# Performance work log

Measured on AMD Instinct MI355X. Metric: run time of the kernel, lower is better.

Reference implementation:

```python
import jax, jax.numpy as jnp
import numpy as np

B, N, IN_DIM, HID = 32, 1024, 128, 64


def setup_inputs() -> dict:
    key = jax.random.key(0)
    ks = jax.random.split(key, 12)
    s_in = 1.0 / np.sqrt(IN_DIM)
    s_h = 1.0 / np.sqrt(HID)
    return {
        "x": jax.random.normal(ks[0], (B, N, IN_DIM), dtype=jnp.float32),
        "A": jax.random.uniform(ks[1], (B, N, N), dtype=jnp.float32),
        # fc_hidden: input_dim -> hidden_dim
        "W_h": jax.random.uniform(ks[2], (IN_DIM, HID), jnp.float32, -s_in, s_in),
        "b_h": jax.random.uniform(ks[3], (HID,), jnp.float32, -s_in, s_in),
        # fc_1 inside Gated_Skip_Connection (input_dim != output_dim)
        "W_fc1": jax.random.uniform(ks[4], (IN_DIM, HID), jnp.float32, -s_in, s_in),
        "b_fc1": jax.random.uniform(ks[5], (HID,), jnp.float32, -s_in, s_in),
        # gated_X1, gated_X2: hidden -> hidden
        "W_g1": jax.random.uniform(ks[6], (HID, HID), jnp.float32, -s_h, s_h),
        "b_g1": jax.random.uniform(ks[7], (HID,), jnp.float32, -s_h, s_h),
        "W_g2": jax.random.uniform(ks[8], (HID, HID), jnp.float32, -s_h, s_h),
        "b_g2": jax.random.uniform(ks[9], (HID,), jnp.float32, -s_h, s_h),
    }


def reference(x, A, W_h, b_h, W_fc1, b_fc1, W_g1, b_g1, W_g2, b_g2):
    # x_new = bmm(A, fc_hidden(x))   [B, N, HID]
    x_new = jnp.einsum("bnm,bmh->bnh", A, x @ W_h + b_h)
    # gated skip connection (input_dim != output_dim -> project x first)
    x_proj = x @ W_fc1 + b_fc1
    gate = jax.nn.sigmoid((x_proj @ W_g1 + b_g1) + (x_new @ W_g2 + b_g2))
    out = x_new * gate + x_proj * (1.0 - gate)
    return out
```

## Files before the change

### kernel.cpp

```cpp
#include <hip/hip_runtime.h>
#include <hip/hip_bf16.h>

#define NB 32
#define NN 1024
#define IND 128
#define HD 64

typedef float f32x4 __attribute__((ext_vector_type(4)));
typedef short bf16x8 __attribute__((ext_vector_type(8)));
typedef unsigned short ushortx4 __attribute__((ext_vector_type(4)));

union FragU { unsigned short us[8]; bf16x8 v; };

__device__ __forceinline__ unsigned short f2bf(float f) {
    union { float f; unsigned u; } x; x.f = f;
    unsigned r = x.u + 0x7FFFu + ((x.u >> 16) & 1u);
    return (unsigned short)(r >> 16);
}
__device__ __forceinline__ float bf2f(unsigned short h) {
    union { unsigned u; float f; } x; x.u = ((unsigned)h) << 16; return x.f;
}

__device__ __forceinline__ void gl16(void* lds, const void* g) {
    __builtin_amdgcn_global_load_lds(
        (const __attribute__((address_space(1))) unsigned int*)g,
        (__attribute__((address_space(3))) unsigned int*)lds, 16, 0, 0);
}

__global__ void prep_k(const float* __restrict__ W_h, const float* __restrict__ W_fc1,
                       const float* __restrict__ W_g1, const float* __restrict__ W_g2,
                       const float* __restrict__ b_g1, const float* __restrict__ b_g2,
                       unsigned short* __restrict__ WcT_hi, unsigned short* __restrict__ WcT_lo,
                       unsigned short* __restrict__ Wg1T_hi, unsigned short* __restrict__ Wg1T_lo,
                       unsigned short* __restrict__ Wg2T_hi, unsigned short* __restrict__ Wg2T_lo,
                       float* __restrict__ biasP1) {
    int t = blockIdx.x * blockDim.x + threadIdx.x;
    if (t < 16384) {
        int o = t >> 7, k = t & 127;
        float v = (o < 64) ? W_h[k * 64 + o] : W_fc1[k * 64 + (o - 64)];
        unsigned short hi = f2bf(v);
        WcT_hi[t] = hi; WcT_lo[t] = f2bf(v - bf2f(hi));
    } else if (t < 20480) {
        int r = t - 16384; int o = r >> 6, k = r & 63;
        float v = W_g1[k * 64 + o];
        unsigned short hi = f2bf(v);
        Wg1T_hi[r] = hi; Wg1T_lo[r] = f2bf(v - bf2f(hi));
    } else if (t < 24576) {
        int r = t - 20480; int o = r >> 6, k = r & 63;
        float v = W_g2[k * 64 + o];
        unsigned short hi = f2bf(v);
        Wg2T_hi[r] = hi; Wg2T_lo[r] = f2bf(v - bf2f(hi));
    } else if (t < 24640) {
        int j = t - 24576;
        biasP1[j] = b_g1[j] + b_g2[j];
    }
}

__global__ __launch_bounds__(64) void k1(
        const float* __restrict__ x,
        const unsigned short* __restrict__ WcT_hi, const unsigned short* __restrict__ WcT_lo,
        const unsigned short* __restrict__ Wg1T_hi, const unsigned short* __restrict__ Wg1T_lo,
        const float* __restrict__ b_h, const float* __restrict__ b_fc1,
        const float* __restrict__ biasP1,
        unsigned short* __restrict__ hF, float* __restrict__ xproj,
        float* __restrict__ p1) {
    __shared__ unsigned short lds_hi[16 * 64];
    __shared__ unsigned short lds_lo[16 * 64];

    const int lane = threadIdx.x;
    const int lr = lane & 15, lg = lane >> 4;
    const int blk = blockIdx.x;
    const int b = blk >> 6;
    const int n0 = (blk & 63) * 16;

    const float* xp = x + (size_t)(b * NN + n0 + lr) * IND;

    f32x4 xa[4][2];
#pragma unroll
    for (int ks = 0; ks < 4; ks++) {
        const f32x4* ap = (const f32x4*)(xp + 32 * ks + 8 * lg);
        xa[ks][0] = ap[0]; xa[ks][1] = ap[1];
    }

    f32x4 acc[8];
#pragma unroll
    for (int f = 0; f < 8; f++) acc[f] = (f32x4){0.f, 0.f, 0.f, 0.f};

#pragma unroll
    for (int ks = 0; ks < 4; ks++) {
        FragU ah, al;
#pragma unroll
        for (int i = 0; i < 4; i++) {
            unsigned short h0 = f2bf(xa[ks][0][i]); ah.us[i] = h0;     al.us[i]     = f2bf(xa[ks][0][i] - bf2f(h0));
            unsigned short h1 = f2bf(xa[ks][1][i]); ah.us[4 + i] = h1; al.us[4 + i] = f2bf(xa[ks][1][i] - bf2f(h1));
        }
#pragma unroll
        for (int f = 0; f < 8; f++) {
            int off = (16 * f + lr) * 128 + 32 * ks + 8 * lg;
            bf16x8 wh = *(const bf16x8*)(WcT_hi + off);
            bf16x8 wl = *(const bf16x8*)(WcT_lo + off);
            acc[f] = __builtin_amdgcn_mfma_f32_16x16x32_bf16(ah.v, wh, acc[f], 0, 0, 0);
            acc[f] = __builtin_amdgcn_mfma_f32_16x16x32_bf16(ah.v, wl, acc[f], 0, 0, 0);
            acc[f] = __builtin_amdgcn_mfma_f32_16x16x32_bf16(al.v, wh, acc[f], 0, 0, 0);
        }
    }

    const int mb = n0 + 4 * lg;
    const int tile = mb >> 5;
    const int lanepart = lr + 16 * ((mb >> 3) & 3);
    const int j0 = mb & 7;

#pragma unroll
    for (int f = 0; f < 4; f++) {
        int c = 16 * f + lr;
        float bh = b_h[c];
        ushortx4 hv;
#pragma unroll
        for (int r = 0; r < 4; r++) hv[r] = f2bf(acc[f][r] + bh);
        *(ushortx4*)(hF + (size_t)b * 65536 + (size_t)(tile * 4 + f) * 512 + lanepart * 8 + j0) = hv;
    }

#pragma unroll
    for (int f = 4; f < 8; f++) {
        int c = 16 * (f - 4) + lr;
        float bp = b_fc1[c];
#pragma unroll
        for (int r = 0; r < 4; r++) {
            float v = acc[f][r] + bp;
            int n = mb + r;
            xproj[(size_t)(b * NN + n) * 64 + c] = v;
            int ln = 4 * lg + r;
            int idx = ln * 64 + (((c >> 3) ^ (ln & 7)) << 3) + (c & 7);
            unsigned short hi = f2bf(v);
            lds_hi[idx] = hi;
            lds_lo[idx] = f2bf(v - bf2f(hi));
        }
    }
    __syncthreads();

    f32x4 accP[4];
#pragma unroll
    for (int f = 0; f < 4; f++) accP[f] = (f32x4){0.f, 0.f, 0.f, 0.f};
#pragma unroll
    for (int ks = 0; ks < 2; ks++) {
        int c0 = 32 * ks + 8 * lg;
        int idx = lr * 64 + (((c0 >> 3) ^ (lr & 7)) << 3);
        bf16x8 a_hi = *(const bf16x8*)(lds_hi + idx);
        bf16x8 a_lo = *(const bf16x8*)(lds_lo + idx);
#pragma unroll
        for (int f = 0; f < 4; f++) {
            int off = (16 * f + lr) * 64 + c0;
            bf16x8 b_hi = *(const bf16x8*)(Wg1T_hi + off);
            bf16x8 b_lo = *(const bf16x8*)(Wg1T_lo + off);
            accP[f] = __builtin_amdgcn_mfma_f32_16x16x32_bf16(a_hi, b_hi, accP[f], 0, 0, 0);
            accP[f] = __builtin_amdgcn_mfma_f32_16x16x32_bf16(a_hi, b_lo, accP[f], 0, 0, 0);
            accP[f] = __builtin_amdgcn_mfma_f32_16x16x32_bf16(a_lo, b_hi, accP[f], 0, 0, 0);
        }
    }
#pragma unroll
    for (int f = 0; f < 4; f++) {
        int c = 16 * f + lr;
        float bb = biasP1[c];
#pragma unroll
        for (int r = 0; r < 4; r++) {
            int n = mb + r;
            p1[(size_t)(b * NN + n) * 64 + c] = accP[f][r] + bb;
        }
    }
}

__global__ __launch_bounds__(256, 4) void k2(
        const float* __restrict__ A, const unsigned short* __restrict__ hF,
        const unsigned short* __restrict__ Wg2T_hi, const unsigned short* __restrict__ Wg2T_lo,
        const float* __restrict__ p1, const float* __restrict__ xproj,
        float* __restrict__ out) {
    __shared__ char smem[32768];

    const int tid = threadIdx.x;
    const int w = tid >> 6, lane = tid & 63;
    const int lr = lane & 15, lg = lane >> 4;

    const int bid = blockIdx.x;
    const int wgid = (bid & 7) * 256 + (bid >> 3);
    const int b = wgid >> 6;
    const int strip = wgid & 63;

    const float* aS[4];
#pragma unroll
    for (int i = 0; i < 4; i++) {
        int rl = w * 4 + i;
        aS[i] = A + (size_t)(b * NN + strip * 16 + rl) * NN + ((lane ^ rl) << 2);
    }
    const unsigned short* hp = hF + (size_t)b * 65536 + w * 512 + lane * 8;

    f32x4 acc = (f32x4){0.f, 0.f, 0.f, 0.f};
    bf16x8 hb[8];

#pragma unroll
    for (int i = 0; i < 4; i++)
        gl16(smem + (w * 4 + i) * 1024, aS[i]);
#pragma unroll
    for (int ks = 0; ks < 8; ks++)
        hb[ks] = *(const bf16x8*)(hp + (size_t)ks * 2048);
    __syncthreads();

#define COMPUTE(ks, Abase)                                                     \
    {                                                                          \
        int g0 = (ks) * 8 + lg * 2;                                            \
        f32x4 a0 = *(const f32x4*)((Abase) + ((g0 ^ lr) << 4));                \
        f32x4 a1 = *(const f32x4*)((Abase) + (((g0 + 1) ^ lr) << 4));          \
        FragU au;                                                              \
        _Pragma("unroll")                                                      \
        for (int ii = 0; ii < 4; ii++) {                                       \
            au.us[ii] = f2bf(a0[ii]); au.us[4 + ii] = f2bf(a1[ii]);            \
        }                                                                      \
        acc = __builtin_amdgcn_mfma_f32_16x16x32_bf16(au.v, hb[ks], acc, 0, 0, 0); \
    }

#pragma unroll
    for (int t = 0; t < 4; t++) {
        const int slot = t & 1;
        const char* Abase = smem + slot * 16384 + lr * 1024;

        if (t < 3) {
#pragma unroll
            for (int i = 0; i < 4; i++)
                gl16(smem + (slot ^ 1) * 16384 + (w * 4 + i) * 1024,
                     aS[i] + (t + 1) * 256);
        }

        COMPUTE(0, Abase) COMPUTE(1, Abase) COMPUTE(2, Abase) COMPUTE(3, Abase)
        if (t < 3) {
#pragma unroll
            for (int ks = 0; ks < 4; ks++)
                hb[ks] = *(const bf16x8*)(hp + (size_t)((t + 1) * 8 + ks) * 2048);
        }
        COMPUTE(4, Abase) COMPUTE(5, Abase) COMPUTE(6, Abase) COMPUTE(7, Abase)
        if (t < 3) {
#pragma unroll
            for (int ks = 4; ks < 8; ks++)
                hb[ks] = *(const bf16x8*)(hp + (size_t)((t + 1) * 8 + ks) * 2048);
        }
        __syncthreads();
    }
#undef COMPUTE

    unsigned short* th = (unsigned short*)smem;
    unsigned short* tl = th + 1024;
    {
        int c = 16 * w + lr;
#pragma unroll
        for (int r = 0; r < 4; r++) {
            int row = 4 * lg + r;
            int idx = row * 64 + (((c >> 3) ^ (row & 7)) << 3) + (c & 7);
            float v = acc[r];
            unsigned short hi = f2bf(v);
            th[idx] = hi;
            tl[idx] = f2bf(v - bf2f(hi));
        }
    }
    __syncthreads();

    f32x4 accG = (f32x4){0.f, 0.f, 0.f, 0.f};
#pragma unroll
    for (int ksk = 0; ksk < 2; ksk++) {
        int c0k = 32 * ksk + 8 * lg;
        int idx = lr * 64 + (((c0k >> 3) ^ (lr & 7)) << 3);
        bf16x8 a_hi = *(const bf16x8*)(th + idx);
        bf16x8 a_lo = *(const bf16x8*)(tl + idx);
        int off = (16 * w + lr) * 64 + c0k;
        bf16x8 b_hi = *(const bf16x8*)(Wg2T_hi + off);
        bf16x8 b_lo = *(const bf16x8*)(Wg2T_lo + off);
        accG = __builtin_amdgcn_mfma_f32_16x16x32_bf16(a_hi, b_hi, accG, 0, 0, 0);
        accG = __builtin_amdgcn_mfma_f32_16x16x32_bf16(a_hi, b_lo, accG, 0, 0, 0);
        accG = __builtin_amdgcn_mfma_f32_16x16x32_bf16(a_lo, b_hi, accG, 0, 0, 0);
    }

    {
        int c = 16 * w + lr;
#pragma unroll
        for (int r = 0; r < 4; r++) {
            int n = strip * 16 + 4 * lg + r;
            size_t g = (size_t)(b * NN + n) * 64 + c;
            float z = p1[g] + accG[r];
            float gate = 1.f / (1.f + __expf(-z));
            float xpv = xproj[g];
            out[g] = acc[r] * gate + xpv * (1.f - gate);
        }
    }
}

extern "C" void kernel_launch(void* const* d_in, const int* in_sizes, int n_in,
                              void* d_out, int out_size, void* d_ws, size_t ws_size,
                              hipStream_t stream) {
    const float* x     = (const float*)d_in[0];
    const float* A     = (const float*)d_in[1];
    const float* W_h   = (const float*)d_in[2];
    const float* b_h   = (const float*)d_in[3];
    const float* W_fc1 = (const float*)d_in[4];
    const float* b_fc1 = (const float*)d_in[5];
    const float* W_g1  = (const float*)d_in[6];
    const float* b_g1  = (const float*)d_in[7];
    const float* W_g2  = (const float*)d_in[8];
    const float* b_g2  = (const float*)d_in[9];
    float* out = (float*)d_out;

    char* ws = (char*)d_ws;
    unsigned short* WcT_hi  = (unsigned short*)(ws);
    unsigned short* WcT_lo  = (unsigned short*)(ws + 32768);
    unsigned short* Wg1T_hi = (unsigned short*)(ws + 65536);
    unsigned short* Wg1T_lo = (unsigned short*)(ws + 73728);
    unsigned short* Wg2T_hi = (unsigned short*)(ws + 81920);
    unsigned short* Wg2T_lo = (unsigned short*)(ws + 90112);
    float*          bP1     = (float*)(ws + 98304);
    unsigned short* hF      = (unsigned short*)(ws + 131072);
    float*          xprj    = (float*)(ws + 131072 + 4194304);
    float*          p1      = (float*)(ws + 131072 + 4194304 + 8388608);

    prep_k<<<97, 256, 0, stream>>>(W_h, W_fc1, W_g1, W_g2, b_g1, b_g2,
                                   WcT_hi, WcT_lo, Wg1T_hi, Wg1T_lo, Wg2T_hi, Wg2T_lo, bP1);
    k1<<<2048, 64, 0, stream>>>(x, WcT_hi, WcT_lo, Wg1T_hi, Wg1T_lo, b_h, b_fc1, bP1,
                                hF, xprj, p1);
    k2<<<2048, 256, 0, stream>>>(A, hF, Wg2T_hi, Wg2T_lo, p1, xprj, out);
}
```

Measured before the change: 63.26 us.

## Load full A strip into LDS upfront instead of double-buffered chunks

Each block now issues all global-to-LDS loads for its 16-row A strip at once into a 64KB shared buffer, removing the per-chunk double-buffering and three of the four barriers. This aims to cut synchronization overhead and expose more memory-level parallelism per block. The trade-off is doubled LDS use and launch bounds lowered to 2 blocks per CU, which reduces occupancy and cross-block latency hiding.

```diff
diff --git a/kernel.cpp b/kernel.cpp
--- a/kernel.cpp
+++ b/kernel.cpp
@@ -169,12 +169,12 @@
     }
 }
 
-__global__ __launch_bounds__(256, 4) void k2(
+__global__ __launch_bounds__(256, 2) void k2(
         const float* __restrict__ A, const unsigned short* __restrict__ hF,
         const unsigned short* __restrict__ Wg2T_hi, const unsigned short* __restrict__ Wg2T_lo,
         const float* __restrict__ p1, const float* __restrict__ xproj,
         float* __restrict__ out) {
-    __shared__ char smem[32768];
+    __shared__ char smem[65536];
 
     const int tid = threadIdx.x;
     const int w = tid >> 6, lane = tid & 63;
@@ -185,65 +185,60 @@
     const int b = wgid >> 6;
     const int strip = wgid & 63;
 
-    const float* aS[4];
 #pragma unroll
     for (int i = 0; i < 4; i++) {
-        int rl = w * 4 + i;
-        aS[i] = A + (size_t)(b * NN + strip * 16 + rl) * NN + ((lane ^ rl) << 2);
-    }
+        const int rl = w * 4 + i;
+        const float* rowp = A + (size_t)(b * NN + strip * 16 + rl) * NN;
+        char* ldsrow = smem + rl * 4096;
+#pragma unroll
+        for (int c = 0; c < 4; c++)
+            gl16(ldsrow + c * 1024, rowp + c * 256 + ((lane ^ rl) << 2));
+    }
+
     const unsigned short* hp = hF + (size_t)b * 65536 + w * 512 + lane * 8;
-
-    f32x4 acc = (f32x4){0.f, 0.f, 0.f, 0.f};
     bf16x8 hb[8];
-
-#pragma unroll
-    for (int i = 0; i < 4; i++)
-        gl16(smem + (w * 4 + i) * 1024, aS[i]);
 #pragma unroll
     for (int ks = 0; ks < 8; ks++)
         hb[ks] = *(const bf16x8*)(hp + (size_t)ks * 2048);
+
     __syncthreads();
 
-#define COMPUTE(ks, Abase)                                                     \
+    f32x4 acc = (f32x4){0.f, 0.f, 0.f, 0.f};
+    const char* Abase = smem + lr * 4096;
+
+#define COMPUTE(KABS, KREG)                                                    \
     {                                                                          \
-        int g0 = (ks) * 8 + lg * 2;                                            \
-        f32x4 a0 = *(const f32x4*)((Abase) + ((g0 ^ lr) << 4));                \
-        f32x4 a1 = *(const f32x4*)((Abase) + (((g0 + 1) ^ lr) << 4));          \
+        int g0 = (KABS) * 8 + lg * 2;                                          \
+        f32x4 a0 = *(const f32x4*)(Abase + ((g0 ^ lr) << 4));                  \
+        f32x4 a1 = *(const f32x4*)(Abase + (((g0 + 1) ^ lr) << 4));            \
         FragU au;                                                              \
         _Pragma("unroll")                                                      \
         for (int ii = 0; ii < 4; ii++) {                                       \
             au.us[ii] = f2bf(a0[ii]); au.us[4 + ii] = f2bf(a1[ii]);            \
         }                                                                      \
-        acc = __builtin_amdgcn_mfma_f32_16x16x32_bf16(au.v, hb[ks], acc, 0, 0, 0); \
+        acc = __builtin_amdgcn_mfma_f32_16x16x32_bf16(au.v, hb[KREG], acc, 0, 0, 0); \
     }
 
 #pragma unroll
     for (int t = 0; t < 4; t++) {
-        const int slot = t & 1;
-        const char* Abase = smem + slot * 16384 + lr * 1024;
-
-        if (t < 3) {
-#pragma unroll
-            for (int i = 0; i < 4; i++)
-                gl16(smem + (slot ^ 1) * 16384 + (w * 4 + i) * 1024,
-                     aS[i] + (t + 1) * 256);
-        }
-
-        COMPUTE(0, Abase) COMPUTE(1, Abase) COMPUTE(2, Abase) COMPUTE(3, Abase)
+        COMPUTE(t * 8 + 0, 0) COMPUTE(t * 8 + 1, 1)
+        COMPUTE(t * 8 + 2, 2) COMPUTE(t * 8 + 3, 3)
         if (t < 3) {
 #pragma unroll
             for (int ks = 0; ks < 4; ks++)
                 hb[ks] = *(const bf16x8*)(hp + (size_t)((t + 1) * 8 + ks) * 2048);
         }
-        COMPUTE(4, Abase) COMPUTE(5, Abase) COMPUTE(6, Abase) COMPUTE(7, Abase)
+        COMPUTE(t * 8 + 4, 4) COMPUTE(t * 8 + 5, 5)
+        COMPUTE(t * 8 + 6, 6) COMPUTE(t * 8 + 7, 7)
         if (t < 3) {
 #pragma unroll
             for (int ks = 4; ks < 8; ks++)
                 hb[ks] = *(const bf16x8*)(hp + (size_t)((t + 1) * 8 + ks) * 2048);
         }
-        __syncthreads();
     }
 #undef COMPUTE
+
+    __syncthreads();
 
     unsigned short* th = (unsigned short*)smem;
     unsigned short* tl = th + 1024;
```

Measured after the change: 71.28 us. 1.13x slower.

## Process two 16-row strips per block in k2 with continuous A prefetch

Applied to the files above, without the earlier changes.

Each k2 workgroup now handles two consecutive 16-row strips of A instead of one, halving the grid to 1024 blocks. The double-buffered A prefetch carries over from the first strip's last tile into the second strip's first tile, so the second strip's load overlaps the first strip's compute and epilogue. The epilogue transpose buffer moves to a separate 4KB LDS region so it doesn't conflict with in-flight prefetches. In exchange the kernel uses more LDS per block, which may reduce occupancy, and has fewer blocks to spread across the CUs.

```diff
diff --git a/kernel.cpp b/kernel.cpp
--- a/kernel.cpp
+++ b/kernel.cpp
@@ -174,26 +174,25 @@
         const unsigned short* __restrict__ Wg2T_hi, const unsigned short* __restrict__ Wg2T_lo,
         const float* __restrict__ p1, const float* __restrict__ xproj,
         float* __restrict__ out) {
-    __shared__ char smem[32768];
+    __shared__ char smem[36864];
 
     const int tid = threadIdx.x;
     const int w = tid >> 6, lane = tid & 63;
     const int lr = lane & 15, lg = lane >> 4;
 
     const int bid = blockIdx.x;
-    const int wgid = (bid & 7) * 256 + (bid >> 3);
-    const int b = wgid >> 6;
-    const int strip = wgid & 63;
+    const int wgid = (bid & 7) * 128 + (bid >> 3);
+    const int b = wgid >> 5;
+    const int blkst = wgid & 31;
 
     const float* aS[4];
 #pragma unroll
     for (int i = 0; i < 4; i++) {
         int rl = w * 4 + i;
-        aS[i] = A + (size_t)(b * NN + strip * 16 + rl) * NN + ((lane ^ rl) << 2);
+        aS[i] = A + (size_t)(b * NN + blkst * 32 + rl) * NN + ((lane ^ rl) << 2);
     }
     const unsigned short* hp = hF + (size_t)b * 65536 + w * 512 + lane * 8;
 
-    f32x4 acc = (f32x4){0.f, 0.f, 0.f, 0.f};
     bf16x8 hb[8];
 
 #pragma unroll
@@ -218,76 +217,84 @@
     }
 
 #pragma unroll
-    for (int t = 0; t < 4; t++) {
-        const int slot = t & 1;
-        const char* Abase = smem + slot * 16384 + lr * 1024;
-
-        if (t < 3) {
-#pragma unroll
-            for (int i = 0; i < 4; i++)
-                gl16(smem + (slot ^ 1) * 16384 + (w * 4 + i) * 1024,
-                     aS[i] + (t + 1) * 256);
-        }
-
-        COMPUTE(0, Abase) COMPUTE(1, Abase) COMPUTE(2, Abase) COMPUTE(3, Abase)
-        if (t < 3) {
-#pragma unroll
-            for (int ks = 0; ks < 4; ks++)
-                hb[ks] = *(const bf16x8*)(hp + (size_t)((t + 1) * 8 + ks) * 2048);
-        }
-        COMPUTE(4, Abase) COMPUTE(5, Abase) COMPUTE(6, Abase) COMPUTE(7, Abase)
-        if (t < 3) {
-#pragma unroll
-            for (int ks = 4; ks < 8; ks++)
-                hb[ks] = *(const bf16x8*)(hp + (size_t)((t + 1) * 8 + ks) * 2048);
+    for (int s = 0; s < 2; s++) {
+        f32x4 acc = (f32x4){0.f, 0.f, 0.f, 0.f};
+
+#pragma unroll
+        for (int t = 0; t < 4; t++) {
+            const char* Abase = smem + (t & 1) * 16384 + lr * 1024;
+            const bool last = (s == 1) && (t == 3);
+            if (!last) {
+                const size_t soff = (t < 3) ? ((size_t)s * 16384 + (t + 1) * 256)
+                                            : ((size_t)(s + 1) * 16384);
+#pragma unroll
+                for (int i = 0; i < 4; i++)
+                    gl16(smem + ((t + 1) & 1) * 16384 + (w * 4 + i) * 1024,
+                         aS[i] + soff);
+            }
+            const int tn = (t < 3) ? (t + 1) : 0;
+
+            COMPUTE(0, Abase) COMPUTE(1, Abase) COMPUTE(2, Abase) COMPUTE(3, Abase)
+            if (!last) {
+#pragma unroll
+                for (int ks = 0; ks < 4; ks++)
+                    hb[ks] = *(const bf16x8*)(hp + (size_t)(tn * 8 + ks) * 2048);
+            }
+            COMPUTE(4, Abase) COMPUTE(5, Abase) COMPUTE(6, Abase) COMPUTE(7, Abase)
+            if (!last) {
+#pragma unroll
+                for (int ks = 4; ks < 8; ks++)
+                    hb[ks] = *(const bf16x8*)(hp + (size_t)(tn * 8 + ks) * 2048);
+            }
+            __syncthreads();
+        }
+
+        unsigned short* th = (unsigned short*)(smem + 32768);
+        unsigned short* tl = th + 1024;
+        {
+            int c = 16 * w + lr;
+#pragma unroll
+            for (int r = 0; r < 4; r++) {
+                int row = 4 * lg + r;
+                int idx = row * 64 + (((c >> 3) ^ (row & 7)) << 3) + (c & 7);
+                float v = acc[r];
+                unsigned short hi = f2bf(v);
+                th[idx] = hi;
+                tl[idx] = f2bf(v - bf2f(hi));
+            }
         }
         __syncthreads();
+
+        f32x4 accG = (f32x4){0.f, 0.f, 0.f, 0.f};
+#pragma unroll
+        for (int ksk = 0; ksk < 2; ksk++) {
+            int c0k = 32 * ksk + 8 * lg;
+            int idx = lr * 64 + (((c0k >> 3) ^ (lr & 7)) << 3);
+            bf16x8 a_hi = *(const bf16x8*)(th + idx);
+            bf16x8 a_lo = *(const bf16x8*)(tl + idx);
+            int off = (16 * w + lr) * 64 + c0k;
+            bf16x8 b_hi = *(const bf16x8*)(Wg2T_hi + off);
+            bf16x8 b_lo = *(const bf16x8*)(Wg2T_lo + off);
+            accG = __builtin_amdgcn_mfma_f32_16x16x32_bf16(a_hi, b_hi, accG, 0, 0, 0);
+            accG = __builtin_amdgcn_mfma_f32_16x16x32_bf16(a_hi, b_lo, accG, 0, 0, 0);
+            accG = __builtin_amdgcn_mfma_f32_16x16x32_bf16(a_lo, b_hi, accG, 0, 0, 0);
+        }
+
+        {
+            int c = 16 * w + lr;
+#pragma unroll
+            for (int r = 0; r < 4; r++) {
+                int n = (blkst * 2 + s) * 16 + 4 * lg + r;
+                size_t g = (size_t)(b * NN + n) * 64 + c;
+                float z = p1[g] + accG[r];
+                float gate = 1.f / (1.f + __expf(-z));
+                float xpv = xproj[g];
+                out[g] = acc[r] * gate + xpv * (1.f - gate);
+            }
+        }
+        __syncthreads();
     }
 #undef COMPUTE
-
-    unsigned short* th = (unsigned short*)smem;
-    unsigned short* tl = th + 1024;
-    {
-        int c = 16 * w + lr;
-#pragma unroll
-        for (int r = 0; r < 4; r++) {
-            int row = 4 * lg + r;
-            int idx = row * 64 + (((c >> 3) ^ (row & 7)) << 3) + (c & 7);
-            float v = acc[r];
-            unsigned short hi = f2bf(v);
-            th[idx] = hi;
-            tl[idx] = f2bf(v - bf2f(hi));
-        }
-    }
-    __syncthreads();
-
-    f32x4 accG = (f32x4){0.f, 0.f, 0.f, 0.f};
-#pragma unroll
-    for (int ksk = 0; ksk < 2; ksk++) {
-        int c0k = 32 * ksk + 8 * lg;
-        int idx = lr * 64 + (((c0k >> 3) ^ (lr & 7)) << 3);
-        bf16x8 a_hi = *(const bf16x8*)(th + idx);
-        bf16x8 a_lo = *(const bf16x8*)(tl + idx);
-        int off = (16 * w + lr) * 64 + c0k;
-        bf16x8 b_hi = *(const bf16x8*)(Wg2T_hi + off);
-        bf16x8 b_lo = *(const bf16x8*)(Wg2T_lo + off);
-        accG = __builtin_amdgcn_mfma_f32_16x16x32_bf16(a_hi, b_hi, accG, 0, 0, 0);
-        accG = __builtin_amdgcn_mfma_f32_16x16x32_bf16(a_hi, b_lo, accG, 0, 0, 0);
-        accG = __builtin_amdgcn_mfma_f32_16x16x32_bf16(a_lo, b_hi, accG, 0, 0, 0);
-    }
-
-    {
-        int c = 16 * w + lr;
-#pragma unroll
-        for (int r = 0; r < 4; r++) {
-            int n = strip * 16 + 4 * lg + r;
-            size_t g = (size_t)(b * NN + n) * 64 + c;
-            float z = p1[g] + accG[r];
-            float gate = 1.f / (1.f + __expf(-z));
-            float xpv = xproj[g];
-            out[g] = acc[r] * gate + xpv * (1.f - gate);
-        }
-    }
 }
 
 extern "C" void kernel_launch(void* const* d_in, const int* in_sizes, int n_in,
@@ -321,5 +328,5 @@
                                    WcT_hi, WcT_lo, Wg1T_hi, Wg1T_lo, Wg2T_hi, Wg2T_lo, bP1);
     k1<<<2048, 64, 0, stream>>>(x, WcT_hi, WcT_lo, Wg1T_hi, Wg1T_lo, b_h, b_fc1, bP1,
                                 hF, xprj, p1);
-    k2<<<2048, 256, 0, stream>>>(A, hF, Wg2T_hi, Wg2T_lo, p1, xprj, out);
-}
+    k2<<<1024, 256, 0, stream>>>(A, hF, Wg2T_hi, Wg2T_lo, p1, xprj, out);
+}
```

After: 63.40 us. No clear change (+0.2%).
